# Kernel optimization log

Measured on AMD Instinct MI355X. Metric: run time of the kernel, lower is better.

The kernel has to match this reference:

```python
import jax, jax.numpy as jnp
import numpy as np

BETA = 0.25

def setup_inputs() -> dict:
    key = jax.random.key(0)
    k1, k2 = jax.random.split(key)
    N, K, D = 262144, 256, 256
    z_e = jax.random.normal(k1, (N, D), dtype=jnp.float32)
    # nn.Embedding init: uniform(-1/K, 1/K)
    emb_weight = jax.random.uniform(k2, (K, D), dtype=jnp.float32, minval=-1.0 / K, maxval=1.0 / K)
    return {"z_e": z_e, "emb_weight": emb_weight}

def reference(z_e, emb_weight):
    # squared L2 distances: ||z||^2 + ||e||^2 - 2 z e^T  -> [N, K]
    dist = (jnp.sum(z_e ** 2, axis=1, keepdims=True)
            + jnp.sum(emb_weight ** 2, axis=1)
            - 2.0 * jnp.matmul(z_e, emb_weight.T))
    encoding_inds = jnp.argmin(dist, axis=1)  # [N]
    z_q = emb_weight[encoding_inds]           # [N, D]

    sg = jax.lax.stop_gradient
    commitment_loss = jnp.mean((sg(z_e) - z_q) ** 2)
    codebook_loss = jnp.mean((z_e - sg(z_q)) ** 2)
    loss = codebook_loss + BETA * commitment_loss

    # straight-through estimator
    z_q_st = z_e + sg(z_q - z_e)
    return z_q_st, encoding_inds, loss
```

## Files before the change

kernel.cpp:

```cpp
#include <hip/hip_runtime.h>

typedef __attribute__((ext_vector_type(8))) short bf16x8;
typedef __attribute__((ext_vector_type(4))) float f32x4;
typedef __attribute__((ext_vector_type(4))) unsigned short us4;
typedef __attribute__((ext_vector_type(8))) unsigned short us8;

#define NROWS 262144
#define KC 256
#define DD 256
#define BM 64
#define DK 32
#define SW 40
#define TAU 3e-4f

__device__ __forceinline__ float np_pw128_sq(const float* a) {
    float r[8];
#pragma unroll
    for (int j = 0; j < 8; ++j) r[j] = __fmul_rn(a[j], a[j]);
    for (int i = 8; i < 128; i += 8) {
#pragma unroll
        for (int j = 0; j < 8; ++j)
            r[j] = __fadd_rn(r[j], __fmul_rn(a[i + j], a[i + j]));
    }
    float t01 = __fadd_rn(r[0], r[1]), t23 = __fadd_rn(r[2], r[3]);
    float t45 = __fadd_rn(r[4], r[5]), t67 = __fadd_rn(r[6], r[7]);
    return __fadd_rn(__fadd_rn(t01, t23), __fadd_rn(t45, t67));
}
__device__ __forceinline__ float np_sum256_sq(const float* a) {
    return __fadd_rn(np_pw128_sq(a), np_pw128_sq(a + 128));
}

__device__ __forceinline__ unsigned cvt_split(float x) {
    unsigned b = __float_as_uint(x);
    unsigned hi = b >> 16;
    float hif = __uint_as_float(b & 0xFFFF0000u);
    float r = x - hif;
    unsigned rb = __float_as_uint(r);
    rb += 0x7FFFu + ((rb >> 16) & 1u);
    return (hi << 16) | (rb >> 16);
}

__global__ void vq_prep(const float* __restrict__ emb, float* __restrict__ se,
                        double* __restrict__ accum) {
    int k = threadIdx.x;
    if (k == 0) *accum = 0.0;
    se[k] = np_sum256_sq(emb + (size_t)k * DD);
}

__global__ void vq_split(const float* __restrict__ emb,
                         unsigned short* __restrict__ ph,
                         unsigned short* __restrict__ pl) {
    int f = (blockIdx.x * 256 + threadIdx.x) * 4;
    float4 v = *reinterpret_cast<const float4*>(emb + f);
    int k = f >> 8, d = f & 255;
    int off = (d >> 5) * (KC * DK) + k * DK + (d & 31);
    unsigned p0 = cvt_split(v.x), p1 = cvt_split(v.y);
    unsigned p2 = cvt_split(v.z), p3 = cvt_split(v.w);
    us4 h, l;
    h[0] = (unsigned short)(p0 >> 16); l[0] = (unsigned short)p0;
    h[1] = (unsigned short)(p1 >> 16); l[1] = (unsigned short)p1;
    h[2] = (unsigned short)(p2 >> 16); l[2] = (unsigned short)p2;
    h[3] = (unsigned short)(p3 >> 16); l[3] = (unsigned short)p3;
    *reinterpret_cast<us4*>(ph + off) = h;
    *reinterpret_cast<us4*>(pl + off) = l;
}

__global__ __launch_bounds__(256, 3)
void vq_main(const float* __restrict__ ze, const float* __restrict__ emb,
             const unsigned short* __restrict__ ph, const unsigned short* __restrict__ pl,
             const float* __restrict__ se_g, float* __restrict__ out_zq,
             float* __restrict__ out_inds, double* __restrict__ accum)
{
    __shared__ __attribute__((aligned(16))) unsigned short zs_hi[BM * SW];
    __shared__ __attribute__((aligned(16))) unsigned short zs_lo[BM * SW];
    __shared__ __attribute__((aligned(16))) unsigned short es_hi[KC * SW];
    __shared__ __attribute__((aligned(16))) unsigned short es_lo[KC * SW];
    __shared__ float  se_s[KC];
    __shared__ int    inds_s[BM];
    __shared__ int    flist[BM];
    __shared__ int    nflag;

    float* wv1 = reinterpret_cast<float*>(es_hi);
    float* wv2 = wv1 + 4 * BM;
    int*   wk1 = reinterpret_cast<int*>(wv2 + 4 * BM);
    float* red   = reinterpret_cast<float*>(es_lo);
    int*   rk2   = reinterpret_cast<int*>(red + 256);
    float* zfull = reinterpret_cast<float*>(rk2 + 256);
    float* srow  = zfull + 256;

    const int t = threadIdx.x;
    const int w = t >> 6;
    const int l = t & 63;
    const int q = (t >> 4) & 3;
    const int c = t & 15;
    const size_t m0 = (size_t)blockIdx.x * BM;

    se_s[t] = se_g[t];
    if (t == 0) nflag = 0;

    f32x4 acc[4][4];
#pragma unroll
    for (int i = 0; i < 4; ++i)
#pragma unroll
        for (int j = 0; j < 4; ++j) acc[i][j] = (f32x4){0.f, 0.f, 0.f, 0.f};
    float sz_acc = 0.f;

    for (int dc = 0; dc < DD; dc += DK) {
        __syncthreads();
        const unsigned short* ehp = ph + (dc >> 5) * (KC * DK);
        const unsigned short* elp = pl + (dc >> 5) * (KC * DK);
#pragma unroll
        for (int it = 0; it < 4; ++it) {
            int idx = it * 256 + t;
            int row = idx >> 2, c8 = idx & 3;
            us8 h = *reinterpret_cast<const us8*>(ehp + idx * 8);
            us8 lo = *reinterpret_cast<const us8*>(elp + idx * 8);
            *reinterpret_cast<us8*>(&es_hi[row * SW + c8 * 8]) = h;
            *reinterpret_cast<us8*>(&es_lo[row * SW + c8 * 8]) = lo;
        }
#pragma unroll
        for (int it = 0; it < 2; ++it) {
            int idx = it * 256 + t;
            int row = idx >> 3, c4 = idx & 7;
            float4 v = *reinterpret_cast<const float4*>(ze + (m0 + row) * DD + dc + c4 * 4);
            sz_acc = fmaf(v.x, v.x, sz_acc); sz_acc = fmaf(v.y, v.y, sz_acc);
            sz_acc = fmaf(v.z, v.z, sz_acc); sz_acc = fmaf(v.w, v.w, sz_acc);
            unsigned p0 = cvt_split(v.x), p1 = cvt_split(v.y);
            unsigned p2 = cvt_split(v.z), p3 = cvt_split(v.w);
            us4 h, lo;
            h[0] = (unsigned short)(p0 >> 16); lo[0] = (unsigned short)p0;
            h[1] = (unsigned short)(p1 >> 16); lo[1] = (unsigned short)p1;
            h[2] = (unsigned short)(p2 >> 16); lo[2] = (unsigned short)p2;
            h[3] = (unsigned short)(p3 >> 16); lo[3] = (unsigned short)p3;
            *reinterpret_cast<us4*>(&zs_hi[row * SW + c4 * 4]) = h;
            *reinterpret_cast<us4*>(&zs_lo[row * SW + c4 * 4]) = lo;
        }
        __syncthreads();
        bf16x8 a_hi[4], a_lo[4], b_hi[4], b_lo[4];
#pragma unroll
        for (int mf = 0; mf < 4; ++mf) {
            a_hi[mf] = *reinterpret_cast<const bf16x8*>(&zs_hi[(16 * mf + c) * SW + q * 8]);
            a_lo[mf] = *reinterpret_cast<const bf16x8*>(&zs_lo[(16 * mf + c) * SW + q * 8]);
        }
#pragma unroll
        for (int nf = 0; nf < 4; ++nf) {
            b_hi[nf] = *reinterpret_cast<const bf16x8*>(&es_hi[(64 * w + 16 * nf + c) * SW + q * 8]);
            b_lo[nf] = *reinterpret_cast<const bf16x8*>(&es_lo[(64 * w + 16 * nf + c) * SW + q * 8]);
        }
#pragma unroll
        for (int mf = 0; mf < 4; ++mf)
#pragma unroll
            for (int nf = 0; nf < 4; ++nf) {
                acc[mf][nf] = __builtin_amdgcn_mfma_f32_16x16x32_bf16(a_lo[mf], b_hi[nf], acc[mf][nf], 0, 0, 0);
                acc[mf][nf] = __builtin_amdgcn_mfma_f32_16x16x32_bf16(a_hi[mf], b_lo[nf], acc[mf][nf], 0, 0, 0);
                acc[mf][nf] = __builtin_amdgcn_mfma_f32_16x16x32_bf16(a_hi[mf], b_hi[nf], acc[mf][nf], 0, 0, 0);
            }
    }
    __syncthreads();

#pragma unroll
    for (int mf = 0; mf < 4; ++mf)
#pragma unroll
        for (int j = 0; j < 4; ++j) {
            float v1 = 3.4e38f, v2 = 3.4e38f; int k1 = 0x7fffffff;
#pragma unroll
            for (int nf = 0; nf < 4; ++nf) {
                int k = 64 * w + 16 * nf + c;
                float dv = fmaf(-2.f, acc[mf][nf][j], se_s[k]);
                if (dv < v1) { v2 = v1; v1 = dv; k1 = k; }
                else if (dv < v2) { v2 = dv; }
            }
#pragma unroll
            for (int off = 1; off < 16; off <<= 1) {
                float ov1 = __shfl_xor(v1, off, 64);
                float ov2 = __shfl_xor(v2, off, 64);
                int   ok1 = __shfl_xor(k1, off, 64);
                bool other = (ov1 < v1) || (ov1 == v1 && ok1 < k1);
                float nv2 = other ? fminf(v1, ov2) : fminf(v2, ov1);
                if (other) { v1 = ov1; k1 = ok1; }
                v2 = nv2;
            }
            if (c == 0) {
                int row = 16 * mf + 4 * q + j;
                wv1[w * BM + row] = v1; wv2[w * BM + row] = v2; wk1[w * BM + row] = k1;
            }
        }
    __syncthreads();

    float lossv = 0.f;
    if (t < BM) {
        float v1 = wv1[t], v2 = wv2[t]; int k1 = wk1[t];
#pragma unroll
        for (int ww = 1; ww < 4; ++ww) {
            float ov1 = wv1[ww * BM + t], ov2 = wv2[ww * BM + t];
            int ok1 = wk1[ww * BM + t];
            bool other = (ov1 < v1) || (ov1 == v1 && ok1 < k1);
            float nv2 = other ? fminf(v1, ov2) : fminf(v2, ov1);
            if (other) { v1 = ov1; k1 = ok1; }
            v2 = nv2;
        }
        inds_s[t] = k1;
        lossv = v1;
        if (v2 - v1 < TAU) {
            int s = atomicAdd(&nflag, 1);
            flist[s] = t;
        }
    }
    __syncthreads();

    int nf = nflag;
    for (int f = 0; f < nf; ++f) {
        int row = flist[f];
        if (t < 64)
            reinterpret_cast<float4*>(zfull)[t] =
                reinterpret_cast<const float4*>(ze + (m0 + row) * DD)[t];
        __syncthreads();
        if (t == 0) *srow = np_sum256_sq(zfull);
        __syncthreads();
        const float4* e4p = reinterpret_cast<const float4*>(emb + (size_t)t * DD);
        float m32 = 0.f;
        for (int d4 = 0; d4 < 64; ++d4) {
            float4 e4 = e4p[d4];
            int d = d4 * 4;
            m32 = __fmaf_rn(zfull[d + 0], e4.x, m32);
            m32 = __fmaf_rn(zfull[d + 1], e4.y, m32);
            m32 = __fmaf_rn(zfull[d + 2], e4.z, m32);
            m32 = __fmaf_rn(zfull[d + 3], e4.w, m32);
        }
        float A  = __fadd_rn(*srow, se_s[t]);
        float Dq = __fsub_rn(A, __fmul_rn(2.0f, m32));
        red[t] = Dq; rk2[t] = t;
        __syncthreads();
        for (int s = 128; s > 0; s >>= 1) {
            if (t < s) {
                float vo = red[t + s]; int ko = rk2[t + s];
                if (vo < red[t] || (vo == red[t] && ko < rk2[t])) { red[t] = vo; rk2[t] = ko; }
            }
            __syncthreads();
        }
        if (t == 0) inds_s[row] = rk2[0];
        __syncthreads();
    }

    if (t < BM) out_inds[m0 + t] = (float)inds_s[t];

    for (int r = w; r < BM; r += 4) {
        int k = inds_s[r];
        float4 v = *reinterpret_cast<const float4*>(emb + (size_t)k * DD + l * 4);
        *reinterpret_cast<float4*>(out_zq + (m0 + r) * DD + l * 4) = v;
    }

    red[t] = sz_acc + lossv;
    __syncthreads();
    for (int s = 128; s > 0; s >>= 1) {
        if (t < s) red[t] += red[t + s];
        __syncthreads();
    }
    if (t == 0) atomicAdd(accum, (double)red[0]);
}

__global__ void vq_fin(const double* __restrict__ accum, float* __restrict__ out_loss) {
    *out_loss = (float)(1.25 * (*accum) / ((double)NROWS * (double)DD));
}

extern "C" void kernel_launch(void* const* d_in, const int* in_sizes, int n_in,
                              void* d_out, int out_size, void* d_ws, size_t ws_size,
                              hipStream_t stream) {
    const float* ze  = (const float*)d_in[0];
    const float* emb = (const float*)d_in[1];
    float* out      = (float*)d_out;
    float* out_zq   = out;
    float* out_inds = out + (size_t)NROWS * DD;
    float* out_loss = out + (size_t)NROWS * DD + NROWS;
    double* accum = (double*)d_ws;
    float*  se    = (float*)((char*)d_ws + 16);
    unsigned short* ph = (unsigned short*)((char*)d_ws + 2048);
    unsigned short* pl = (unsigned short*)((char*)d_ws + 2048 + 131072);

    vq_prep<<<1, 256, 0, stream>>>(emb, se, accum);
    vq_split<<<KC * DD / (256 * 4), 256, 0, stream>>>(emb, ph, pl);
    vq_main<<<NROWS / BM, 256, 0, stream>>>(ze, emb, ph, pl, se, out_zq, out_inds, accum);
    vq_fin<<<1, 1, 0, stream>>>(accum, out_loss);
}
```

Measured before the change: 349.0 us.

## Drop z low-part MFMA, prefetch z chunks, move near-tie rescoring to separate kernel

The z operand is now only truncated to bf16 hi (no lo split), so one of the three split-bf16 MFMAs per tile and the z_lo shared buffer go away, with the tie threshold TAU raised to cover the larger error. The next z chunk is loaded into registers before the barrier to overlap global latency with the MFMA work. Near-tie rows are appended to a global list and rescored in exact fp32 by a new vq_fix kernel, instead of serially inside each block. The list is capped at FCAP entries, so if more rows are flagged the extras are never rescored and could get wrong indices.

```diff
diff --git a/kernel.cpp b/kernel.cpp
--- a/kernel.cpp
+++ b/kernel.cpp
@@ -11,7 +11,8 @@
 #define BM 64
 #define DK 32
 #define SW 40
-#define TAU 3e-4f
+#define TAU 1e-3f
+#define FCAP 32768
 
 __device__ __forceinline__ float np_pw128_sq(const float* a) {
     float r[8];
@@ -41,9 +42,9 @@
 }
 
 __global__ void vq_prep(const float* __restrict__ emb, float* __restrict__ se,
-                        double* __restrict__ accum) {
+                        double* __restrict__ accum, int* __restrict__ gcnt) {
     int k = threadIdx.x;
-    if (k == 0) *accum = 0.0;
+    if (k == 0) { *accum = 0.0; *gcnt = 0; }
     se[k] = np_sum256_sq(emb + (size_t)k * DD);
 }
 
@@ -69,24 +70,19 @@
 void vq_main(const float* __restrict__ ze, const float* __restrict__ emb,
              const unsigned short* __restrict__ ph, const unsigned short* __restrict__ pl,
              const float* __restrict__ se_g, float* __restrict__ out_zq,
-             float* __restrict__ out_inds, double* __restrict__ accum)
+             float* __restrict__ out_inds, double* __restrict__ accum,
+             int* __restrict__ glist, int* __restrict__ gcnt)
 {
     __shared__ __attribute__((aligned(16))) unsigned short zs_hi[BM * SW];
-    __shared__ __attribute__((aligned(16))) unsigned short zs_lo[BM * SW];
     __shared__ __attribute__((aligned(16))) unsigned short es_hi[KC * SW];
     __shared__ __attribute__((aligned(16))) unsigned short es_lo[KC * SW];
     __shared__ float  se_s[KC];
     __shared__ int    inds_s[BM];
-    __shared__ int    flist[BM];
-    __shared__ int    nflag;
 
     float* wv1 = reinterpret_cast<float*>(es_hi);
     float* wv2 = wv1 + 4 * BM;
     int*   wk1 = reinterpret_cast<int*>(wv2 + 4 * BM);
-    float* red   = reinterpret_cast<float*>(es_lo);
-    int*   rk2   = reinterpret_cast<int*>(red + 256);
-    float* zfull = reinterpret_cast<float*>(rk2 + 256);
-    float* srow  = zfull + 256;
+    float* red = reinterpret_cast<float*>(es_lo);
 
     const int t = threadIdx.x;
     const int w = t >> 6;
@@ -94,9 +90,9 @@
     const int q = (t >> 4) & 3;
     const int c = t & 15;
     const size_t m0 = (size_t)blockIdx.x * BM;
+    const float* zbase = ze + m0 * DD;
 
     se_s[t] = se_g[t];
-    if (t == 0) nflag = 0;
 
     f32x4 acc[4][4];
 #pragma unroll
@@ -105,7 +101,15 @@
         for (int j = 0; j < 4; ++j) acc[i][j] = (f32x4){0.f, 0.f, 0.f, 0.f};
     float sz_acc = 0.f;
 
-    for (int dc = 0; dc < DD; dc += DK) {
+    const int i0 = t, i1 = 256 + t;
+    const int r0 = i0 >> 3, c40 = i0 & 7;
+    const int r1 = i1 >> 3, c41 = i1 & 7;
+
+    float4 zva = *reinterpret_cast<const float4*>(zbase + (size_t)r0 * DD + 0 + c40 * 4);
+    float4 zvb = *reinterpret_cast<const float4*>(zbase + (size_t)r1 * DD + 0 + c41 * 4);
+
+    for (int dci = 0; dci < 8; ++dci) {
+        const int dc = dci * DK;
         __syncthreads();
         const unsigned short* ehp = ph + (dc >> 5) * (KC * DK);
         const unsigned short* elp = pl + (dc >> 5) * (KC * DK);
@@ -113,35 +117,40 @@
         for (int it = 0; it < 4; ++it) {
             int idx = it * 256 + t;
             int row = idx >> 2, c8 = idx & 3;
-            us8 h = *reinterpret_cast<const us8*>(ehp + idx * 8);
+            us8 h  = *reinterpret_cast<const us8*>(ehp + idx * 8);
             us8 lo = *reinterpret_cast<const us8*>(elp + idx * 8);
             *reinterpret_cast<us8*>(&es_hi[row * SW + c8 * 8]) = h;
             *reinterpret_cast<us8*>(&es_lo[row * SW + c8 * 8]) = lo;
         }
-#pragma unroll
-        for (int it = 0; it < 2; ++it) {
-            int idx = it * 256 + t;
-            int row = idx >> 3, c4 = idx & 7;
-            float4 v = *reinterpret_cast<const float4*>(ze + (m0 + row) * DD + dc + c4 * 4);
-            sz_acc = fmaf(v.x, v.x, sz_acc); sz_acc = fmaf(v.y, v.y, sz_acc);
-            sz_acc = fmaf(v.z, v.z, sz_acc); sz_acc = fmaf(v.w, v.w, sz_acc);
-            unsigned p0 = cvt_split(v.x), p1 = cvt_split(v.y);
-            unsigned p2 = cvt_split(v.z), p3 = cvt_split(v.w);
-            us4 h, lo;
-            h[0] = (unsigned short)(p0 >> 16); lo[0] = (unsigned short)p0;
-            h[1] = (unsigned short)(p1 >> 16); lo[1] = (unsigned short)p1;
-            h[2] = (unsigned short)(p2 >> 16); lo[2] = (unsigned short)p2;
-            h[3] = (unsigned short)(p3 >> 16); lo[3] = (unsigned short)p3;
-            *reinterpret_cast<us4*>(&zs_hi[row * SW + c4 * 4]) = h;
-            *reinterpret_cast<us4*>(&zs_lo[row * SW + c4 * 4]) = lo;
-        }
-        __syncthreads();
-        bf16x8 a_hi[4], a_lo[4], b_hi[4], b_lo[4];
-#pragma unroll
-        for (int mf = 0; mf < 4; ++mf) {
+        {
+            sz_acc = fmaf(zva.x, zva.x, sz_acc); sz_acc = fmaf(zva.y, zva.y, sz_acc);
+            sz_acc = fmaf(zva.z, zva.z, sz_acc); sz_acc = fmaf(zva.w, zva.w, sz_acc);
+            us4 h;
+            h[0] = (unsigned short)(__float_as_uint(zva.x) >> 16);
+            h[1] = (unsigned short)(__float_as_uint(zva.y) >> 16);
+            h[2] = (unsigned short)(__float_as_uint(zva.z) >> 16);
+            h[3] = (unsigned short)(__float_as_uint(zva.w) >> 16);
+            *reinterpret_cast<us4*>(&zs_hi[r0 * SW + c40 * 4]) = h;
+        }
+        {
+            sz_acc = fmaf(zvb.x, zvb.x, sz_acc); sz_acc = fmaf(zvb.y, zvb.y, sz_acc);
+            sz_acc = fmaf(zvb.z, zvb.z, sz_acc); sz_acc = fmaf(zvb.w, zvb.w, sz_acc);
+            us4 h;
+            h[0] = (unsigned short)(__float_as_uint(zvb.x) >> 16);
+            h[1] = (unsigned short)(__float_as_uint(zvb.y) >> 16);
+            h[2] = (unsigned short)(__float_as_uint(zvb.z) >> 16);
+            h[3] = (unsigned short)(__float_as_uint(zvb.w) >> 16);
+            *reinterpret_cast<us4*>(&zs_hi[r1 * SW + c41 * 4]) = h;
+        }
+        if (dci < 7) {
+            zva = *reinterpret_cast<const float4*>(zbase + (size_t)r0 * DD + dc + DK + c40 * 4);
+            zvb = *reinterpret_cast<const float4*>(zbase + (size_t)r1 * DD + dc + DK + c41 * 4);
+        }
+        __syncthreads();
+        bf16x8 a_hi[4], b_hi[4], b_lo[4];
+#pragma unroll
+        for (int mf = 0; mf < 4; ++mf)
             a_hi[mf] = *reinterpret_cast<const bf16x8*>(&zs_hi[(16 * mf + c) * SW + q * 8]);
-            a_lo[mf] = *reinterpret_cast<const bf16x8*>(&zs_lo[(16 * mf + c) * SW + q * 8]);
-        }
 #pragma unroll
         for (int nf = 0; nf < 4; ++nf) {
             b_hi[nf] = *reinterpret_cast<const bf16x8*>(&es_hi[(64 * w + 16 * nf + c) * SW + q * 8]);
@@ -151,7 +160,6 @@
         for (int mf = 0; mf < 4; ++mf)
 #pragma unroll
             for (int nf = 0; nf < 4; ++nf) {
-                acc[mf][nf] = __builtin_amdgcn_mfma_f32_16x16x32_bf16(a_lo[mf], b_hi[nf], acc[mf][nf], 0, 0, 0);
                 acc[mf][nf] = __builtin_amdgcn_mfma_f32_16x16x32_bf16(a_hi[mf], b_lo[nf], acc[mf][nf], 0, 0, 0);
                 acc[mf][nf] = __builtin_amdgcn_mfma_f32_16x16x32_bf16(a_hi[mf], b_hi[nf], acc[mf][nf], 0, 0, 0);
             }
@@ -202,61 +210,78 @@
         inds_s[t] = k1;
         lossv = v1;
         if (v2 - v1 < TAU) {
-            int s = atomicAdd(&nflag, 1);
-            flist[s] = t;
+            int s = atomicAdd(gcnt, 1);
+            if (s < FCAP) glist[s] = (int)(m0 + t);
         }
     }
     __syncthreads();
 
-    int nf = nflag;
-    for (int f = 0; f < nf; ++f) {
-        int row = flist[f];
+    if (t < BM) out_inds[m0 + t] = (float)inds_s[t];
+
+    for (int r = w; r < BM; r += 4) {
+        int k = inds_s[r];
+        float4 v = *reinterpret_cast<const float4*>(emb + (size_t)k * DD + l * 4);
+        *reinterpret_cast<float4*>(out_zq + (m0 + r) * DD + l * 4) = v;
+    }
+
+    red[t] = sz_acc + lossv;
+    __syncthreads();
+    for (int s = 128; s > 0; s >>= 1) {
+        if (t < s) red[t] += red[t + s];
+        __syncthreads();
+    }
+    if (t == 0) atomicAdd(accum, (double)red[0]);
+}
+
+__global__ __launch_bounds__(256)
+void vq_fix(const float* __restrict__ ze, const float* __restrict__ emb,
+            const float* __restrict__ se_g, const int* __restrict__ glist,
+            const int* __restrict__ gcnt, float* __restrict__ out_zq,
+            float* __restrict__ out_inds)
+{
+    __shared__ float zf[256];
+    __shared__ float srow;
+    __shared__ float red[256];
+    __shared__ int   rk[256];
+
+    const int t = threadIdx.x;
+    int F = *gcnt; if (F > FCAP) F = FCAP;
+    const float se_k = se_g[t];
+    const float4* e4p = reinterpret_cast<const float4*>(emb + (size_t)t * DD);
+
+    for (int i = blockIdx.x; i < F; i += gridDim.x) {
+        int row = glist[i];
+        __syncthreads();
         if (t < 64)
-            reinterpret_cast<float4*>(zfull)[t] =
-                reinterpret_cast<const float4*>(ze + (m0 + row) * DD)[t];
-        __syncthreads();
-        if (t == 0) *srow = np_sum256_sq(zfull);
-        __syncthreads();
-        const float4* e4p = reinterpret_cast<const float4*>(emb + (size_t)t * DD);
+            reinterpret_cast<float4*>(zf)[t] =
+                reinterpret_cast<const float4*>(ze + (size_t)row * DD)[t];
+        __syncthreads();
+        if (t == 0) srow = np_sum256_sq(zf);
+        __syncthreads();
         float m32 = 0.f;
         for (int d4 = 0; d4 < 64; ++d4) {
             float4 e4 = e4p[d4];
             int d = d4 * 4;
-            m32 = __fmaf_rn(zfull[d + 0], e4.x, m32);
-            m32 = __fmaf_rn(zfull[d + 1], e4.y, m32);
-            m32 = __fmaf_rn(zfull[d + 2], e4.z, m32);
-            m32 = __fmaf_rn(zfull[d + 3], e4.w, m32);
-        }
-        float A  = __fadd_rn(*srow, se_s[t]);
+            m32 = __fmaf_rn(zf[d + 0], e4.x, m32);
+            m32 = __fmaf_rn(zf[d + 1], e4.y, m32);
+            m32 = __fmaf_rn(zf[d + 2], e4.z, m32);
+            m32 = __fmaf_rn(zf[d + 3], e4.w, m32);
+        }
+        float A  = __fadd_rn(srow, se_k);
         float Dq = __fsub_rn(A, __fmul_rn(2.0f, m32));
-        red[t] = Dq; rk2[t] = t;
+        red[t] = Dq; rk[t] = t;
         __syncthreads();
         for (int s = 128; s > 0; s >>= 1) {
             if (t < s) {
-                float vo = red[t + s]; int ko = rk2[t + s];
-                if (vo < red[t] || (vo == red[t] && ko < rk2[t])) { red[t] = vo; rk2[t] = ko; }
+                float vo = red[t + s]; int ko = rk[t + s];
+                if (vo < red[t] || (vo == red[t] && ko < rk[t])) { red[t] = vo; rk[t] = ko; }
             }
             __syncthreads();
         }
-        if (t == 0) inds_s[row] = rk2[0];
-        __syncthreads();
-    }
-
-    if (t < BM) out_inds[m0 + t] = (float)inds_s[t];
-
-    for (int r = w; r < BM; r += 4) {
-        int k = inds_s[r];
-        float4 v = *reinterpret_cast<const float4*>(emb + (size_t)k * DD + l * 4);
-        *reinterpret_cast<float4*>(out_zq + (m0 + r) * DD + l * 4) = v;
-    }
-
-    red[t] = sz_acc + lossv;
-    __syncthreads();
-    for (int s = 128; s > 0; s >>= 1) {
-        if (t < s) red[t] += red[t + s];
-        __syncthreads();
-    }
-    if (t == 0) atomicAdd(accum, (double)red[0]);
+        int kk = rk[0];
+        if (t == 0) out_inds[row] = (float)kk;
+        out_zq[(size_t)row * DD + t] = emb[(size_t)kk * DD + t];
+    }
 }
 
 __global__ void vq_fin(const double* __restrict__ accum, float* __restrict__ out_loss) {
@@ -272,13 +297,18 @@
     float* out_zq   = out;
     float* out_inds = out + (size_t)NROWS * DD;
     float* out_loss = out + (size_t)NROWS * DD + NROWS;
+
     double* accum = (double*)d_ws;
-    float*  se    = (float*)((char*)d_ws + 16);
-    unsigned short* ph = (unsigned short*)((char*)d_ws + 2048);
-    unsigned short* pl = (unsigned short*)((char*)d_ws + 2048 + 131072);
-
-    vq_prep<<<1, 256, 0, stream>>>(emb, se, accum);
+    int*    gcnt  = (int*)((char*)d_ws + 8);
+    float*  se    = (float*)((char*)d_ws + 256);
+    int*    glist = (int*)((char*)d_ws + 4096);
+    unsigned short* ph = (unsigned short*)((char*)d_ws + 4096 + 131072);
+    unsigned short* pl = (unsigned short*)((char*)d_ws + 4096 + 131072 + 131072);
+
+    vq_prep<<<1, 256, 0, stream>>>(emb, se, accum, gcnt);
     vq_split<<<KC * DD / (256 * 4), 256, 0, stream>>>(emb, ph, pl);
-    vq_main<<<NROWS / BM, 256, 0, stream>>>(ze, emb, ph, pl, se, out_zq, out_inds, accum);
+    vq_main<<<NROWS / BM, 256, 0, stream>>>(ze, emb, ph, pl, se, out_zq, out_inds,
+                                            accum, glist, gcnt);
+    vq_fix<<<2048, 256, 0, stream>>>(ze, emb, se, glist, gcnt, out_zq, out_inds);
     vq_fin<<<1, 1, 0, stream>>>(accum, out_loss);
 }
```

New measurement: 555.4 us. 59.1% more time.
